# Kernel optimization log

Hardware: AMD Instinct MI355X
Metric: run time of the kernel (lower is better)

## Reference

```python
import jax, jax.numpy as jnp
import numpy as np

H, KV, D, HID = 16, 4, 64, 1024
OUT_MIN, OUT_MAX = 32, 8192  # output_size_max = config.max_position_embeddings


def _score_attn(x, Wq, Wk, Wv, Wo):
    # Full (non-causal, unmasked) GQA attention whose o_proj maps to 1 scalar/token.
    B, S, _ = x.shape
    q = (x @ Wq).reshape(B, S, H, D)
    k = jnp.repeat((x @ Wk).reshape(B, S, KV, D), H // KV, axis=2)  # repeat_kv
    v = jnp.repeat((x @ Wv).reshape(B, S, KV, D), H // KV, axis=2)
    scores = jnp.einsum('bqhd,bkhd->bhqk', q, k) / jnp.asarray(np.sqrt(D), x.dtype)
    a = jax.nn.softmax(scores, axis=-1)
    o = jnp.einsum('bhqk,bkhd->bqhd', a, v).reshape(B, S, H * D)
    return o @ Wo  # (B, S, 1)


def _dynamic_sizes(x, Wq, Wk, Wv, Wo, scale):
    s = _score_attn(x, Wq, Wk, Wv, Wo)               # (B,S,1)
    means = jax.nn.sigmoid(s).mean(axis=1)            # (B,1) (no attention_mask)
    sizes = means.squeeze(-1) * scale * (OUT_MAX - OUT_MIN) + OUT_MIN
    return sizes.astype(jnp.int32)                    # torch .int() truncation


def _segment_ids(sizes_np, S, max_len):
    # torch.linspace(0, L, sz+1).long() boundaries; token t -> segment i with
    # intervals[i] <= t < intervals[i+1]; right-aligned into [max_len] per batch.
    B = len(sizes_np)
    seg = np.zeros((B, S), np.int32)
    t = np.arange(S)
    for b, sz in enumerate(sizes_np):
        sz = int(sz)
        bnd = np.floor(np.linspace(0.0, S, sz + 1, dtype=np.float64)).astype(np.int64)
        s = np.clip(np.searchsorted(bnd, t, side='right') - 1, 0, sz - 1)
        seg[b] = b * max_len + (max_len - sz) + s
    return jnp.asarray(seg)


def setup_inputs() -> dict:
    key = jax.random.key(0)
    ks = jax.random.split(key, 10)
    B, S = 4, 2048
    x = jax.random.normal(ks[0], (B, S, HID), jnp.float32)
    def lin(k, i, o):
        return jax.random.normal(k, (i, o), jnp.float32) / np.sqrt(i).astype(np.float32)
    return dict(
        hidden_states=x,
        Wq1=lin(ks[1], HID, H * D), Wk1=lin(ks[2], HID, KV * D),
        Wv1=lin(ks[3], HID, KV * D), Wo1=lin(ks[4], H * D, 1),
        Wq2=lin(ks[5], HID, H * D), Wk2=lin(ks[6], HID, KV * D),
        Wv2=lin(ks[7], HID, KV * D), Wo2=lin(ks[8], H * D, 1),
        scale_param=jnp.asarray(0.01, jnp.float32),
    )


def reference(hidden_states, Wq1, Wk1, Wv1, Wo1, Wq2, Wk2, Wv2, Wo2, scale_param):
    B, S, Hd = hidden_states.shape
    # 1) size-estimation attention -> per-batch dynamic output sizes (data-dependent shape)
    sizes = _dynamic_sizes(hidden_states, Wq1, Wk1, Wv1, Wo1, scale_param)
    sizes_np = np.asarray(jax.device_get(sizes))
    max_len = int(sizes_np.max())
    seg = _segment_ids(sizes_np, S, max_len)          # (B,S) global segment ids
    # 2) weighted-pooling attention -> per-token sigmoid weights
    w = jax.nn.sigmoid(_score_attn(hidden_states, Wq2, Wk2, Wv2, Wo2)).squeeze(-1)  # (B,S)
    # 3) weighted average pooling over dynamic-size segments (vectorized scatter-add)
    num = jax.ops.segment_sum((hidden_states * w[..., None]).reshape(B * S, Hd),
                              seg.reshape(-1), num_segments=B * max_len)
    den = jax.ops.segment_sum(w.reshape(-1), seg.reshape(-1), num_segments=B * max_len)
    pooled = (num / (den[:, None] + 1e-8)).reshape(B, max_len, Hd)
    out_mask = jnp.arange(max_len)[None, :] >= (max_len - sizes)[:, None]
    return pooled, out_mask, sizes
```

## Files before the change

### kernel.cpp

```cpp
#include <hip/hip_runtime.h>
#include <math.h>

#define TB 256

constexpr int B_ = 4, S_ = 2048, HID_ = 1024, H_ = 16, KV_ = 4, D_ = 64;

typedef short sh8 __attribute__((ext_vector_type(8)));
typedef float fl4 __attribute__((ext_vector_type(4)));
typedef unsigned short u16;
typedef unsigned int u32;

__device__ __forceinline__ u16 f2bf(float f) {
  u32 u = __float_as_uint(f);
  u += 0x7fff + ((u >> 16) & 1);
  return (u16)(u >> 16);
}
__device__ __forceinline__ float bf2f(u16 h) { return __uint_as_float(((u32)h) << 16); }

constexpr size_t XSZ   = (size_t)B_ * S_ * HID_;
constexpr size_t WQH_O = 2 * XSZ;
constexpr size_t WQSZ  = (size_t)2 * HID_ * (H_ * D_);
constexpr size_t WQL_O = WQH_O + WQSZ;
constexpr size_t WKH_O = WQH_O + 2 * WQSZ;
constexpr size_t WKSZ  = (size_t)2 * HID_ * (KV_ * D_);
constexpr size_t WKL_O = WKH_O + WKSZ;
constexpr size_t KH_O  = WKH_O + 2 * WKSZ;
constexpr size_t KSZ   = (size_t)2 * B_ * KV_ * S_ * D_;
constexpr size_t KL_O  = KH_O + KSZ;
constexpr size_t KPLANE = (size_t)S_ * D_;
constexpr size_t FBASE   = (KH_O + 2 * KSZ) / 2;
constexpr size_t U_OFF   = FBASE;
constexpr size_t U_SZ    = (size_t)2 * B_ * H_ * S_;
constexpr size_t WVO_OFF = U_OFF + U_SZ;
constexpr size_t WVO_SZ  = (size_t)HID_ * 32;
constexpr size_t SH_OFF  = WVO_OFF + WVO_SZ;
constexpr size_t SH_SZ   = (size_t)2 * B_ * S_ * H_;
constexpr size_t W_OFF   = SH_OFF + SH_SZ;
constexpr size_t W_SZ    = (size_t)B_ * S_;
constexpr size_t SUM_OFF = W_OFF + W_SZ;
constexpr size_t SIZES_OFF = SUM_OFF + 8;

__global__ __launch_bounds__(TB) void conv_x_kernel(
    const float* __restrict__ x, float* __restrict__ ws) {
  u16* XH = (u16*)ws;
  u16* XL = XH + XSZ;
  int bt = blockIdx.x;
  int tid = threadIdx.x, w = tid >> 6, lane = tid & 63, quad = lane >> 4, col = lane & 15;
  int b = bt >> 7, t16 = bt & 127;
  const float* row = x + ((size_t)b * S_ + t16 * 16 + col) * HID_;
#pragma unroll
  for (int i = 0; i < 8; ++i) {
    int cs = w + i * 4;
    const float* src = row + cs * 32 + quad * 8;
    float4 v0 = *reinterpret_cast<const float4*>(src);
    float4 v1 = *reinterpret_cast<const float4*>(src + 4);
    float vv[8] = {v0.x, v0.y, v0.z, v0.w, v1.x, v1.y, v1.z, v1.w};
    sh8 hh, ll;
#pragma unroll
    for (int j = 0; j < 8; ++j) {
      u16 hb = f2bf(vv[j]);
      hh[j] = (short)hb;
      ll[j] = (short)f2bf(vv[j] - bf2f(hb));
    }
    size_t fb = ((size_t)bt * 32 + cs) * 512 + (size_t)lane * 8;
    *reinterpret_cast<sh8*>(XH + fb) = hh;
    *reinterpret_cast<sh8*>(XL + fb) = ll;
  }
}

__global__ __launch_bounds__(TB) void conv_w_kernel(
    const float* __restrict__ W1, const float* __restrict__ W2,
    u16* __restrict__ OH, u16* __restrict__ OL, int ncols) {
  __shared__ float wt[32][257];
  int ngrp = ncols >> 8;
  int blk = blockIdx.x;
  int a = blk / (32 * ngrp);
  int rem = blk - a * 32 * ngrp;
  int cs = rem / ngrp, ng = rem - cs * ngrp;
  const float* W = a ? W2 : W1;
  int tid = threadIdx.x;
#pragma unroll
  for (int i = 0; i < 8; ++i) {
    int e = tid + i * 256;
    int r = e >> 6, c4 = (e & 63) * 4;
    float4 v = *reinterpret_cast<const float4*>(
        W + ((size_t)(cs * 32 + r)) * ncols + ng * 256 + c4);
    wt[r][c4] = v.x; wt[r][c4 + 1] = v.y; wt[r][c4 + 2] = v.z; wt[r][c4 + 3] = v.w;
  }
  __syncthreads();
  int w = tid >> 6, lane = tid & 63, quad = lane >> 4, col = lane & 15;
  int NF = ncols >> 4;
#pragma unroll
  for (int f = 0; f < 4; ++f) {
    int n16 = w * 4 + f;
    sh8 hh, ll;
#pragma unroll
    for (int j = 0; j < 8; ++j) {
      float v = wt[quad * 8 + j][n16 * 16 + col];
      u16 hb = f2bf(v);
      hh[j] = (short)hb;
      ll[j] = (short)f2bf(v - bf2f(hb));
    }
    size_t fb = (((size_t)a * 32 + cs) * NF + ng * 16 + n16) * 512 + (size_t)lane * 8;
    *reinterpret_cast<sh8*>(OH + fb) = hh;
    *reinterpret_cast<sh8*>(OL + fb) = ll;
  }
}

__global__ __launch_bounds__(TB) void wvo_kernel(
    const float* __restrict__ Wv1, const float* __restrict__ Wo1,
    const float* __restrict__ Wv2, const float* __restrict__ Wo2,
    float* __restrict__ ws) {
  int n = blockIdx.x;
  int a = n >> 4, h = n & 15, kv = h >> 2;
  const float* Wv = a ? Wv2 : Wv1;
  const float* Wo = a ? Wo2 : Wo1;
  for (int c = threadIdx.x; c < HID_; c += TB) {
    const float* vr = Wv + (size_t)c * (KV_ * D_) + kv * D_;
    const float* wo = Wo + h * D_;
    float acc = 0.f;
#pragma unroll 16
    for (int d = 0; d < D_; ++d) acc += vr[d] * wo[d];
    ws[WVO_OFF + (size_t)c * 32 + n] = acc;
  }
}

__global__ __launch_bounds__(TB) void k_gemm_kernel(float* __restrict__ ws) {
  __shared__ __align__(16) float xs[64][68];
  int k0 = blockIdx.x * 64;
  int kv = blockIdx.y;
  int ab = blockIdx.z, a = ab >> 2, b = ab & 3;
  int tid = threadIdx.x, w = tid >> 6, lane = tid & 63, quad = lane >> 4, col = lane & 15;
  const u16* XH = (const u16*)ws;
  const u16* XL = XH + XSZ;
  const u16* WKH = XH + WKH_O;
  const u16* WKL = XH + WKL_O;
  int tq = (w & 1) * 2, nq = (w >> 1) * 2;
  fl4 C[2][2] = {};
#pragma unroll 2
  for (int cs = 0; cs < 32; ++cs) {
    sh8 ah[2], al[2], bh[2], bl[2];
#pragma unroll
    for (int ti = 0; ti < 2; ++ti) {
      size_t fb = (((size_t)b * 128 + (k0 >> 4) + tq + ti) * 32 + cs) * 512 + (size_t)lane * 8;
      ah[ti] = *reinterpret_cast<const sh8*>(XH + fb);
      if (a == 0) al[ti] = *reinterpret_cast<const sh8*>(XL + fb);
    }
#pragma unroll
    for (int ni = 0; ni < 2; ++ni) {
      size_t fb = (((size_t)a * 32 + cs) * 16 + kv * 4 + nq + ni) * 512 + (size_t)lane * 8;
      bh[ni] = *reinterpret_cast<const sh8*>(WKH + fb);
      if (a == 0) bl[ni] = *reinterpret_cast<const sh8*>(WKL + fb);
    }
#pragma unroll
    for (int ti = 0; ti < 2; ++ti)
#pragma unroll
      for (int ni = 0; ni < 2; ++ni) {
        C[ti][ni] = __builtin_amdgcn_mfma_f32_16x16x32_bf16(ah[ti], bh[ni], C[ti][ni], 0, 0, 0);
        if (a == 0) {
          C[ti][ni] = __builtin_amdgcn_mfma_f32_16x16x32_bf16(al[ti], bh[ni], C[ti][ni], 0, 0, 0);
          C[ti][ni] = __builtin_amdgcn_mfma_f32_16x16x32_bf16(ah[ti], bl[ni], C[ti][ni], 0, 0, 0);
        }
      }
  }
#pragma unroll
  for (int ti = 0; ti < 2; ++ti)
#pragma unroll
    for (int ni = 0; ni < 2; ++ni)
#pragma unroll
      for (int r = 0; r < 4; ++r)
        xs[(tq + ti) * 16 + quad * 4 + r][(nq + ni) * 16 + col] = C[ti][ni][r];
  __syncthreads();
  u16* KH = (u16*)ws + KH_O;
  u16* KL = (u16*)ws + KL_O;
  size_t plane = (size_t)((a * B_ + b) * KV_ + kv) * KPLANE;
#pragma unroll
  for (int t = 0; t < 2; ++t) {
    int f = w + t * 4;
    int k16 = f & 3, ds = f >> 2;
    const float* row = &xs[k16 * 16 + col][ds * 32 + quad * 8];
    sh8 hh, ll;
#pragma unroll
    for (int j = 0; j < 8; ++j) {
      float v = row[j];
      u16 hb = f2bf(v);
      hh[j] = (short)hb;
      ll[j] = (short)f2bf(v - bf2f(hb));
    }
    size_t fb = plane + ((size_t)(((k0 >> 4) + k16) * 2 + ds)) * 512 + (size_t)lane * 8;
    *reinterpret_cast<sh8*>(KH + fb) = hh;
    if (a == 0) *reinterpret_cast<sh8*>(KL + fb) = ll;
  }
}

__global__ __launch_bounds__(TB) void u_gemm_kernel(
    const float* __restrict__ x, float* __restrict__ ws) {
  __shared__ float xs[64][68];
  __shared__ float uw[64][36];
  int k0 = blockIdx.x * 64, b = blockIdx.y;
  int tid = threadIdx.x;
  int tk = tid >> 2, ng = tid & 3;
  int lr = tid >> 4, lc4 = (tid & 15) * 4;
  float acc[8] = {};
  for (int c0 = 0; c0 < HID_; c0 += 64) {
    __syncthreads();
#pragma unroll
    for (int p = 0; p < 4; ++p) {
      int r = lr + p * 16;
      *reinterpret_cast<float4*>(&xs[r][lc4]) =
          *reinterpret_cast<const float4*>(x + ((size_t)(b * S_ + k0 + r) * HID_ + c0 + lc4));
    }
    {
      int cc = tid >> 3, n4 = (tid & 7) * 4;
      *reinterpret_cast<float4*>(&uw[cc][n4]) =
          *reinterpret_cast<const float4*>(ws + WVO_OFF + (size_t)(c0 + cc) * 32 + n4);
      *reinterpret_cast<float4*>(&uw[cc + 32][n4]) =
          *reinterpret_cast<const float4*>(ws + WVO_OFF + (size_t)(c0 + cc + 32) * 32 + n4);
    }
    __syncthreads();
#pragma unroll 8
    for (int cc = 0; cc < 64; ++cc) {
      float xv = xs[tk][cc];
      float4 a0 = *reinterpret_cast<const float4*>(&uw[cc][ng * 8]);
      float4 a1 = *reinterpret_cast<const float4*>(&uw[cc][ng * 8 + 4]);
      acc[0] += xv * a0.x; acc[1] += xv * a0.y; acc[2] += xv * a0.z; acc[3] += xv * a0.w;
      acc[4] += xv * a1.x; acc[5] += xv * a1.y; acc[6] += xv * a1.z; acc[7] += xv * a1.w;
    }
  }
#pragma unroll
  for (int j = 0; j < 8; ++j) {
    int n = ng * 8 + j, a = n >> 4, h = n & 15;
    ws[U_OFF + ((size_t)(a * B_ + b) * H_ + h) * S_ + k0 + tk] = acc[j];
  }
}

__global__ __launch_bounds__(TB) void attn_kernel(float* __restrict__ ws) {
  __shared__ __align__(16) float Qt[64][68];
  __shared__ __align__(16) u16 kbuf[16 * 512];
  int q0 = blockIdx.x * 64;
  int ah = blockIdx.y, a = ah >> 4, h = ah & 15, kv = h >> 2;
  int b = blockIdx.z;
  int tid = threadIdx.x, w = tid >> 6, lane = tid & 63, quad = lane >> 4, col = lane & 15;
  const u16* XH = (const u16*)ws;
  const u16* XL = XH + XSZ;
  const u16* WQH = XH + WQH_O;
  const u16* WQL = XH + WQL_O;

  {
    int tq = (w & 1) * 2, nq = (w >> 1) * 2;
    fl4 C[2][2] = {};
#pragma unroll 2
    for (int cs = 0; cs < 32; ++cs) {
      sh8 ah_[2], al_[2], bh_[2], bl_[2];
#pragma unroll
      for (int ti = 0; ti < 2; ++ti) {
        size_t fb = (((size_t)b * 128 + (q0 >> 4) + tq + ti) * 32 + cs) * 512 + (size_t)lane * 8;
        ah_[ti] = *reinterpret_cast<const sh8*>(XH + fb);
        if (a == 0) al_[ti] = *reinterpret_cast<const sh8*>(XL + fb);
      }
#pragma unroll
      for (int ni = 0; ni < 2; ++ni) {
        size_t fb = (((size_t)a * 32 + cs) * 64 + h * 4 + nq + ni) * 512 + (size_t)lane * 8;
        bh_[ni] = *reinterpret_cast<const sh8*>(WQH + fb);
        if (a == 0) bl_[ni] = *reinterpret_cast<const sh8*>(WQL + fb);
      }
#pragma unroll
      for (int ti = 0; ti < 2; ++ti)
#pragma unroll
        for (int ni = 0; ni < 2; ++ni) {
          C[ti][ni] = __builtin_amdgcn_mfma_f32_16x16x32_bf16(ah_[ti], bh_[ni], C[ti][ni], 0, 0, 0);
          if (a == 0) {
            C[ti][ni] = __builtin_amdgcn_mfma_f32_16x16x32_bf16(al_[ti], bh_[ni], C[ti][ni], 0, 0, 0);
            C[ti][ni] = __builtin_amdgcn_mfma_f32_16x16x32_bf16(ah_[ti], bl_[ni], C[ti][ni], 0, 0, 0);
          }
        }
    }
#pragma unroll
    for (int ti = 0; ti < 2; ++ti)
#pragma unroll
      for (int ni = 0; ni < 2; ++ni)
#pragma unroll
        for (int r = 0; r < 4; ++r)
          Qt[(nq + ni) * 16 + col][(tq + ti) * 16 + quad * 4 + r] = C[ti][ni][r];
  }
  __syncthreads();

  sh8 qh[2], ql[2];
#pragma unroll
  for (int ds = 0; ds < 2; ++ds)
#pragma unroll
    for (int j = 0; j < 8; ++j) {
      float v = Qt[ds * 32 + quad * 8 + j][w * 16 + col];
      u16 hb = f2bf(v);
      qh[ds][j] = (short)hb;
      if (a == 0) ql[ds][j] = (short)f2bf(v - bf2f(hb));
    }

  const u16* KHg = (const u16*)ws + KH_O + (size_t)((a * B_ + b) * KV_ + kv) * KPLANE;
  const u16* KLg = (const u16*)ws + KL_O + (size_t)((a * B_ + b) * KV_ + kv) * KPLANE;
  const float* Ug = ws + U_OFF + ((size_t)(a * B_ + b) * H_ + h) * S_;
  int nld = (a == 0) ? 4 : 2;
  float num[4] = {}, den[4] = {};
  for (int k0 = 0; k0 < S_; k0 += 64) {
    __syncthreads();
#pragma unroll
    for (int i = 0; i < 4; ++i) {
      if (i < nld) {
        int c = tid + TB * i, f = c >> 6, ln = c & 63;
        const u16* src;
        if (a == 0) {
          int st = f >> 2, ds = (f >> 1) & 1, p = f & 1;
          src = (p ? KLg : KHg) + ((size_t)(((k0 >> 4) + st) * 2 + ds)) * 512 + (size_t)ln * 8;
        } else {
          int st = f >> 1, ds = f & 1;
          src = KHg + ((size_t)(((k0 >> 4) + st) * 2 + ds)) * 512 + (size_t)ln * 8;
        }
        *reinterpret_cast<uint4*>(kbuf + (size_t)c * 8) = *reinterpret_cast<const uint4*>(src);
      }
    }
    __syncthreads();
    const sh8* kb = (const sh8*)kbuf;
#pragma unroll
    for (int st = 0; st < 4; ++st) {
      sh8 bh0, bh1, bl0, bl1;
      if (a == 0) {
        bh0 = kb[(st * 4 + 0) * 64 + lane];
        bl0 = kb[(st * 4 + 1) * 64 + lane];
        bh1 = kb[(st * 4 + 2) * 64 + lane];
        bl1 = kb[(st * 4 + 3) * 64 + lane];
      } else {
        bh0 = kb[(st * 2 + 0) * 64 + lane];
        bh1 = kb[(st * 2 + 1) * 64 + lane];
      }
      fl4 C = {0.f, 0.f, 0.f, 0.f};
      C = __builtin_amdgcn_mfma_f32_16x16x32_bf16(qh[0], bh0, C, 0, 0, 0);
      C = __builtin_amdgcn_mfma_f32_16x16x32_bf16(qh[1], bh1, C, 0, 0, 0);
      if (a == 0) {
        C = __builtin_amdgcn_mfma_f32_16x16x32_bf16(ql[0], bh0, C, 0, 0, 0);
        C = __builtin_amdgcn_mfma_f32_16x16x32_bf16(ql[1], bh1, C, 0, 0, 0);
        C = __builtin_amdgcn_mfma_f32_16x16x32_bf16(qh[0], bl0, C, 0, 0, 0);
        C = __builtin_amdgcn_mfma_f32_16x16x32_bf16(qh[1], bl1, C, 0, 0, 0);
      }
      float uval = Ug[k0 + st * 16 + col];
#pragma unroll
      for (int r = 0; r < 4; ++r) {
        float e = __expf(C[r] * 0.125f);
        den[r] += e;
        num[r] += e * uval;
      }
    }
  }
#pragma unroll
  for (int off = 1; off < 16; off <<= 1)
#pragma unroll
    for (int r = 0; r < 4; ++r) {
      den[r] += __shfl_xor(den[r], off);
      num[r] += __shfl_xor(num[r], off);
    }
  if (col == 0) {
#pragma unroll
    for (int r = 0; r < 4; ++r) {
      int q = q0 + w * 16 + quad * 4 + r;
      ws[SH_OFF + ((size_t)(a * B_ + b) * S_ + q) * H_ + h] = num[r] / den[r];
    }
  }
}

__global__ __launch_bounds__(TB) void post_kernel(float* __restrict__ ws) {
  int g = blockIdx.x * TB + threadIdx.x;
  int b = g >> 11, q = g & (S_ - 1);
  const float* sh = ws + SH_OFF;
  float s1 = 0.f, s2 = 0.f;
#pragma unroll
  for (int h = 0; h < H_; ++h) {
    s1 += sh[((size_t)b * S_ + q) * H_ + h];
    s2 += sh[((size_t)(B_ + b) * S_ + q) * H_ + h];
  }
  ws[W_OFF + g] = 1.f / (1.f + expf(-s2));
  double sig = 1.0 / (1.0 + exp(-(double)s1));
#pragma unroll
  for (int off = 1; off < 64; off <<= 1) sig += __shfl_xor(sig, off);
  __shared__ double red[4];
  int tid = threadIdx.x;
  if ((tid & 63) == 0) red[tid >> 6] = sig;
  __syncthreads();
  if (tid == 0)
    atomicAdd(reinterpret_cast<double*>(ws + SUM_OFF) + b,
              red[0] + red[1] + red[2] + red[3]);
}

__global__ void sizes_kernel(const float* __restrict__ scale_p, float* __restrict__ ws,
                             float* __restrict__ out_sizes) {
  int b = threadIdx.x;
  if (b < B_) {
    double m = reinterpret_cast<const double*>(ws + SUM_OFF)[b] / (double)S_;
    double v = m * (double)(*scale_p) * (double)(8192 - 32) + 32.0;
    int sz = (int)v;
    reinterpret_cast<int*>(ws + SIZES_OFF)[b] = sz;
    out_sizes[b] = (float)sz;
  }
}

__global__ __launch_bounds__(TB) void pool_kernel(
    const float* __restrict__ x, const float* __restrict__ ws,
    float* __restrict__ out, int max_len) {
  int p = blockIdx.x, b = blockIdx.y;
  int sz = reinterpret_cast<const int*>(ws + SIZES_OFF)[b];
  int s = p - (max_len - sz);
  int tid = threadIdx.x;
  size_t obase = ((size_t)b * max_len + p) * HID_;
  size_t maskbase = (size_t)B_ * max_len * HID_;
  if (s < 0) {
    *reinterpret_cast<float4*>(out + obase + tid * 4) = make_float4(0.f, 0.f, 0.f, 0.f);
    if (tid == 0) out[maskbase + (size_t)b * max_len + p] = 0.f;
    return;
  }
  double step = (double)S_ / (double)sz;
  int t0 = (int)floor((double)s * step);
  int t1 = (s + 1 == sz) ? S_ : (int)floor((double)(s + 1) * step);
  const float* wv = ws + W_OFF + (size_t)b * S_;
  const float* xb = x + (size_t)b * S_ * HID_;
  float den = 0.f, acc0 = 0.f, acc1 = 0.f, acc2 = 0.f, acc3 = 0.f;
  for (int t = t0; t < t1; ++t) {
    float wt = wv[t];
    den += wt;
    float4 xv = *reinterpret_cast<const float4*>(xb + (size_t)t * HID_ + tid * 4);
    acc0 += xv.x * wt; acc1 += xv.y * wt; acc2 += xv.z * wt; acc3 += xv.w * wt;
  }
  float d = den + 1e-8f;
  *reinterpret_cast<float4*>(out + obase + tid * 4) =
      make_float4(acc0 / d, acc1 / d, acc2 / d, acc3 / d);
  if (tid == 0) out[maskbase + (size_t)b * max_len + p] = 1.f;
}

extern "C" void kernel_launch(void* const* d_in, const int* in_sizes, int n_in,
                              void* d_out, int out_size, void* d_ws, size_t ws_size,
                              hipStream_t stream) {
  const float* x    = (const float*)d_in[0];
  const float* Wq1  = (const float*)d_in[1];
  const float* Wk1  = (const float*)d_in[2];
  const float* Wv1  = (const float*)d_in[3];
  const float* Wo1  = (const float*)d_in[4];
  const float* Wq2  = (const float*)d_in[5];
  const float* Wk2  = (const float*)d_in[6];
  const float* Wv2  = (const float*)d_in[7];
  const float* Wo2  = (const float*)d_in[8];
  const float* scale = (const float*)d_in[9];
  float* ws  = (float*)d_ws;
  u16* wsu   = (u16*)d_ws;
  float* out = (float*)d_out;

  int max_len = (out_size - B_) / (B_ * (HID_ + 1));

  hipMemsetAsync((void*)(ws + SUM_OFF), 0, 4 * sizeof(double), stream);
  conv_x_kernel<<<B_ * (S_ / 16), TB, 0, stream>>>(x, ws);
  conv_w_kernel<<<2 * 32 * 4, TB, 0, stream>>>(Wq1, Wq2, wsu + WQH_O, wsu + WQL_O, H_ * D_);
  conv_w_kernel<<<2 * 32 * 1, TB, 0, stream>>>(Wk1, Wk2, wsu + WKH_O, wsu + WKL_O, KV_ * D_);
  wvo_kernel<<<32, TB, 0, stream>>>(Wv1, Wo1, Wv2, Wo2, ws);
  k_gemm_kernel<<<dim3(S_ / 64, KV_, 8), TB, 0, stream>>>(ws);
  u_gemm_kernel<<<dim3(S_ / 64, B_), TB, 0, stream>>>(x, ws);
  attn_kernel<<<dim3(S_ / 64, 32, B_), TB, 0, stream>>>(ws);
  post_kernel<<<(B_ * S_) / TB, TB, 0, stream>>>(ws);
  float* out_sizes = out + (size_t)B_ * max_len * HID_ + (size_t)B_ * max_len;
  sizes_kernel<<<1, 64, 0, stream>>>(scale, ws, out_sizes);
  pool_kernel<<<dim3(max_len, B_), TB, 0, stream>>>(x, ws, out, max_len);
}
```

Baseline: 510.7 us.

## Merge prep kernels into two launches, fold sizes into pool, hoist attn addressing

```diff
diff --git a/kernel.cpp b/kernel.cpp
--- a/kernel.cpp
+++ b/kernel.cpp
@@ -38,47 +38,16 @@
 constexpr size_t W_OFF   = SH_OFF + SH_SZ;
 constexpr size_t W_SZ    = (size_t)B_ * S_;
 constexpr size_t SUM_OFF = W_OFF + W_SZ;
-constexpr size_t SIZES_OFF = SUM_OFF + 8;
-
-__global__ __launch_bounds__(TB) void conv_x_kernel(
-    const float* __restrict__ x, float* __restrict__ ws) {
-  u16* XH = (u16*)ws;
-  u16* XL = XH + XSZ;
-  int bt = blockIdx.x;
-  int tid = threadIdx.x, w = tid >> 6, lane = tid & 63, quad = lane >> 4, col = lane & 15;
-  int b = bt >> 7, t16 = bt & 127;
-  const float* row = x + ((size_t)b * S_ + t16 * 16 + col) * HID_;
-#pragma unroll
-  for (int i = 0; i < 8; ++i) {
-    int cs = w + i * 4;
-    const float* src = row + cs * 32 + quad * 8;
-    float4 v0 = *reinterpret_cast<const float4*>(src);
-    float4 v1 = *reinterpret_cast<const float4*>(src + 4);
-    float vv[8] = {v0.x, v0.y, v0.z, v0.w, v1.x, v1.y, v1.z, v1.w};
-    sh8 hh, ll;
-#pragma unroll
-    for (int j = 0; j < 8; ++j) {
-      u16 hb = f2bf(vv[j]);
-      hh[j] = (short)hb;
-      ll[j] = (short)f2bf(vv[j] - bf2f(hb));
-    }
-    size_t fb = ((size_t)bt * 32 + cs) * 512 + (size_t)lane * 8;
-    *reinterpret_cast<sh8*>(XH + fb) = hh;
-    *reinterpret_cast<sh8*>(XL + fb) = ll;
-  }
-}
-
-__global__ __launch_bounds__(TB) void conv_w_kernel(
+
+__device__ __forceinline__ void conv_w_body(
     const float* __restrict__ W1, const float* __restrict__ W2,
-    u16* __restrict__ OH, u16* __restrict__ OL, int ncols) {
-  __shared__ float wt[32][257];
+    u16* __restrict__ OH, u16* __restrict__ OL, int ncols,
+    int blk, int tid, float wt[32][257]) {
   int ngrp = ncols >> 8;
-  int blk = blockIdx.x;
   int a = blk / (32 * ngrp);
   int rem = blk - a * 32 * ngrp;
   int cs = rem / ngrp, ng = rem - cs * ngrp;
   const float* W = a ? W2 : W1;
-  int tid = threadIdx.x;
 #pragma unroll
   for (int i = 0; i < 8; ++i) {
     int e = tid + i * 256;
@@ -107,136 +76,173 @@
   }
 }
 
-__global__ __launch_bounds__(TB) void wvo_kernel(
+__global__ __launch_bounds__(TB) void prep1_kernel(
+    const float* __restrict__ x,
+    const float* __restrict__ Wq1, const float* __restrict__ Wq2,
+    const float* __restrict__ Wk1, const float* __restrict__ Wk2,
     const float* __restrict__ Wv1, const float* __restrict__ Wo1,
     const float* __restrict__ Wv2, const float* __restrict__ Wo2,
     float* __restrict__ ws) {
-  int n = blockIdx.x;
-  int a = n >> 4, h = n & 15, kv = h >> 2;
-  const float* Wv = a ? Wv2 : Wv1;
-  const float* Wo = a ? Wo2 : Wo1;
-  for (int c = threadIdx.x; c < HID_; c += TB) {
-    const float* vr = Wv + (size_t)c * (KV_ * D_) + kv * D_;
-    const float* wo = Wo + h * D_;
-    float acc = 0.f;
+  __shared__ float wt[32][257];
+  int blk = blockIdx.x, tid = threadIdx.x;
+  u16* wsu = (u16*)ws;
+  if (blk < 512) {
+    u16* XH = wsu;
+    u16* XL = XH + XSZ;
+    int bt = blk;
+    int w = tid >> 6, lane = tid & 63, quad = lane >> 4, col = lane & 15;
+    int b = bt >> 7, t16 = bt & 127;
+    const float* row = x + ((size_t)b * S_ + t16 * 16 + col) * HID_;
+#pragma unroll
+    for (int i = 0; i < 8; ++i) {
+      int cs = w + i * 4;
+      const float* src = row + cs * 32 + quad * 8;
+      float4 v0 = *reinterpret_cast<const float4*>(src);
+      float4 v1 = *reinterpret_cast<const float4*>(src + 4);
+      float vv[8] = {v0.x, v0.y, v0.z, v0.w, v1.x, v1.y, v1.z, v1.w};
+      sh8 hh, ll;
+#pragma unroll
+      for (int j = 0; j < 8; ++j) {
+        u16 hb = f2bf(vv[j]);
+        hh[j] = (short)hb;
+        ll[j] = (short)f2bf(vv[j] - bf2f(hb));
+      }
+      size_t fb = ((size_t)bt * 32 + cs) * 512 + (size_t)lane * 8;
+      *reinterpret_cast<sh8*>(XH + fb) = hh;
+      *reinterpret_cast<sh8*>(XL + fb) = ll;
+    }
+  } else if (blk < 768) {
+    conv_w_body(Wq1, Wq2, wsu + WQH_O, wsu + WQL_O, H_ * D_, blk - 512, tid, wt);
+  } else if (blk < 832) {
+    conv_w_body(Wk1, Wk2, wsu + WKH_O, wsu + WKL_O, KV_ * D_, blk - 768, tid, wt);
+  } else {
+    int n = blk - 832, a = n >> 4, h = n & 15, kv = h >> 2;
+    const float* Wv = a ? Wv2 : Wv1;
+    const float* Wo = a ? Wo2 : Wo1;
+    for (int c = tid; c < HID_; c += TB) {
+      const float* vr = Wv + (size_t)c * (KV_ * D_) + kv * D_;
+      const float* wo = Wo + h * D_;
+      float acc = 0.f;
 #pragma unroll 16
-    for (int d = 0; d < D_; ++d) acc += vr[d] * wo[d];
-    ws[WVO_OFF + (size_t)c * 32 + n] = acc;
-  }
-}
-
-__global__ __launch_bounds__(TB) void k_gemm_kernel(float* __restrict__ ws) {
+      for (int d = 0; d < D_; ++d) acc += vr[d] * wo[d];
+      ws[WVO_OFF + (size_t)c * 32 + n] = acc;
+    }
+  }
+}
+
+__global__ __launch_bounds__(TB) void prep2_kernel(
+    const float* __restrict__ x, float* __restrict__ ws) {
   __shared__ __align__(16) float xs[64][68];
-  int k0 = blockIdx.x * 64;
-  int kv = blockIdx.y;
-  int ab = blockIdx.z, a = ab >> 2, b = ab & 3;
-  int tid = threadIdx.x, w = tid >> 6, lane = tid & 63, quad = lane >> 4, col = lane & 15;
-  const u16* XH = (const u16*)ws;
-  const u16* XL = XH + XSZ;
-  const u16* WKH = XH + WKH_O;
-  const u16* WKL = XH + WKL_O;
-  int tq = (w & 1) * 2, nq = (w >> 1) * 2;
-  fl4 C[2][2] = {};
+  __shared__ float uw[64][36];
+  int blk = blockIdx.x, tid = threadIdx.x;
+  if (blk < 1024) {
+    int k0 = (blk & 31) * 64;
+    int kv = (blk >> 5) & 3;
+    int ab = blk >> 7, a = ab >> 2, b = ab & 3;
+    int w = tid >> 6, lane = tid & 63, quad = lane >> 4, col = lane & 15;
+    const u16* XH = (const u16*)ws;
+    const u16* XL = XH + XSZ;
+    const u16* WKH = XH + WKH_O;
+    const u16* WKL = XH + WKL_O;
+    int tq = (w & 1) * 2, nq = (w >> 1) * 2;
+    fl4 C[2][2] = {};
 #pragma unroll 2
-  for (int cs = 0; cs < 32; ++cs) {
-    sh8 ah[2], al[2], bh[2], bl[2];
-#pragma unroll
-    for (int ti = 0; ti < 2; ++ti) {
-      size_t fb = (((size_t)b * 128 + (k0 >> 4) + tq + ti) * 32 + cs) * 512 + (size_t)lane * 8;
-      ah[ti] = *reinterpret_cast<const sh8*>(XH + fb);
-      if (a == 0) al[ti] = *reinterpret_cast<const sh8*>(XL + fb);
-    }
-#pragma unroll
-    for (int ni = 0; ni < 2; ++ni) {
-      size_t fb = (((size_t)a * 32 + cs) * 16 + kv * 4 + nq + ni) * 512 + (size_t)lane * 8;
-      bh[ni] = *reinterpret_cast<const sh8*>(WKH + fb);
-      if (a == 0) bl[ni] = *reinterpret_cast<const sh8*>(WKL + fb);
+    for (int cs = 0; cs < 32; ++cs) {
+      sh8 ah[2], al[2], bh[2], bl[2];
+#pragma unroll
+      for (int ti = 0; ti < 2; ++ti) {
+        size_t fb = (((size_t)b * 128 + (k0 >> 4) + tq + ti) * 32 + cs) * 512 + (size_t)lane * 8;
+        ah[ti] = *reinterpret_cast<const sh8*>(XH + fb);
+        if (a == 0) al[ti] = *reinterpret_cast<const sh8*>(XL + fb);
+      }
+#pragma unroll
+      for (int ni = 0; ni < 2; ++ni) {
+        size_t fb = (((size_t)a * 32 + cs) * 16 + kv * 4 + nq + ni) * 512 + (size_t)lane * 8;
+        bh[ni] = *reinterpret_cast<const sh8*>(WKH + fb);
+        if (a == 0) bl[ni] = *reinterpret_cast<const sh8*>(WKL + fb);
+      }
+#pragma unroll
+      for (int ti = 0; ti < 2; ++ti)
+#pragma unroll
+        for (int ni = 0; ni < 2; ++ni) {
+          C[ti][ni] = __builtin_amdgcn_mfma_f32_16x16x32_bf16(ah[ti], bh[ni], C[ti][ni], 0, 0, 0);
+          if (a == 0) {
+            C[ti][ni] = __builtin_amdgcn_mfma_f32_16x16x32_bf16(al[ti], bh[ni], C[ti][ni], 0, 0, 0);
+            C[ti][ni] = __builtin_amdgcn_mfma_f32_16x16x32_bf16(ah[ti], bl[ni], C[ti][ni], 0, 0, 0);
+          }
+        }
     }
 #pragma unroll
     for (int ti = 0; ti < 2; ++ti)
 #pragma unroll
-      for (int ni = 0; ni < 2; ++ni) {
-        C[ti][ni] = __builtin_amdgcn_mfma_f32_16x16x32_bf16(ah[ti], bh[ni], C[ti][ni], 0, 0, 0);
-        if (a == 0) {
-          C[ti][ni] = __builtin_amdgcn_mfma_f32_16x16x32_bf16(al[ti], bh[ni], C[ti][ni], 0, 0, 0);
-          C[ti][ni] = __builtin_amdgcn_mfma_f32_16x16x32_bf16(ah[ti], bl[ni], C[ti][ni], 0, 0, 0);
-        }
-      }
-  }
-#pragma unroll
-  for (int ti = 0; ti < 2; ++ti)
-#pragma unroll
-    for (int ni = 0; ni < 2; ++ni)
-#pragma unroll
-      for (int r = 0; r < 4; ++r)
-        xs[(tq + ti) * 16 + quad * 4 + r][(nq + ni) * 16 + col] = C[ti][ni][r];
-  __syncthreads();
-  u16* KH = (u16*)ws + KH_O;
-  u16* KL = (u16*)ws + KL_O;
-  size_t plane = (size_t)((a * B_ + b) * KV_ + kv) * KPLANE;
-#pragma unroll
-  for (int t = 0; t < 2; ++t) {
-    int f = w + t * 4;
-    int k16 = f & 3, ds = f >> 2;
-    const float* row = &xs[k16 * 16 + col][ds * 32 + quad * 8];
-    sh8 hh, ll;
+      for (int ni = 0; ni < 2; ++ni)
+#pragma unroll
+        for (int r = 0; r < 4; ++r)
+          xs[(tq + ti) * 16 + quad * 4 + r][(nq + ni) * 16 + col] = C[ti][ni][r];
+    __syncthreads();
+    u16* KH = (u16*)ws + KH_O;
+    u16* KL = (u16*)ws + KL_O;
+    size_t plane = (size_t)((a * B_ + b) * KV_ + kv) * KPLANE;
+#pragma unroll
+    for (int t = 0; t < 2; ++t) {
+      int f = w + t * 4;
+      int k16 = f & 3, ds = f >> 2;
+      const float* row = &xs[k16 * 16 + col][ds * 32 + quad * 8];
+      sh8 hh, ll;
+#pragma unroll
+      for (int j = 0; j < 8; ++j) {
+        float v = row[j];
+        u16 hb = f2bf(v);
+        hh[j] = (short)hb;
+        ll[j] = (short)f2bf(v - bf2f(hb));
+      }
+      size_t fb = plane + ((size_t)(((k0 >> 4) + k16) * 2 + ds)) * 512 + (size_t)lane * 8;
+      *reinterpret_cast<sh8*>(KH + fb) = hh;
+      if (a == 0) *reinterpret_cast<sh8*>(KL + fb) = ll;
+    }
+  } else {
+    int i = blk - 1024;
+    int k0 = (i & 31) * 64, b = i >> 5;
+    int tk = tid >> 2, ng = tid & 3;
+    int lr = tid >> 4, lc4 = (tid & 15) * 4;
+    float acc[8] = {};
+    for (int c0 = 0; c0 < HID_; c0 += 64) {
+      __syncthreads();
+#pragma unroll
+      for (int p = 0; p < 4; ++p) {
+        int r = lr + p * 16;
+        *reinterpret_cast<float4*>(&xs[r][lc4]) =
+            *reinterpret_cast<const float4*>(x + ((size_t)(b * S_ + k0 + r) * HID_ + c0 + lc4));
+      }
+      {
+        int cc = tid >> 3, n4 = (tid & 7) * 4;
+        *reinterpret_cast<float4*>(&uw[cc][n4]) =
+            *reinterpret_cast<const float4*>(ws + WVO_OFF + (size_t)(c0 + cc) * 32 + n4);
+        *reinterpret_cast<float4*>(&uw[cc + 32][n4]) =
+            *reinterpret_cast<const float4*>(ws + WVO_OFF + (size_t)(c0 + cc + 32) * 32 + n4);
+      }
+      __syncthreads();
+#pragma unroll 8
+      for (int cc = 0; cc < 64; ++cc) {
+        float xv = xs[tk][cc];
+        float4 a0 = *reinterpret_cast<const float4*>(&uw[cc][ng * 8]);
+        float4 a1 = *reinterpret_cast<const float4*>(&uw[cc][ng * 8 + 4]);
+        acc[0] += xv * a0.x; acc[1] += xv * a0.y; acc[2] += xv * a0.z; acc[3] += xv * a0.w;
+        acc[4] += xv * a1.x; acc[5] += xv * a1.y; acc[6] += xv * a1.z; acc[7] += xv * a1.w;
+      }
+    }
 #pragma unroll
     for (int j = 0; j < 8; ++j) {
-      float v = row[j];
-      u16 hb = f2bf(v);
-      hh[j] = (short)hb;
-      ll[j] = (short)f2bf(v - bf2f(hb));
-    }
-    size_t fb = plane + ((size_t)(((k0 >> 4) + k16) * 2 + ds)) * 512 + (size_t)lane * 8;
-    *reinterpret_cast<sh8*>(KH + fb) = hh;
-    if (a == 0) *reinterpret_cast<sh8*>(KL + fb) = ll;
-  }
-}
-
-__global__ __launch_bounds__(TB) void u_gemm_kernel(
-    const float* __restrict__ x, float* __restrict__ ws) {
-  __shared__ float xs[64][68];
-  __shared__ float uw[64][36];
-  int k0 = blockIdx.x * 64, b = blockIdx.y;
-  int tid = threadIdx.x;
-  int tk = tid >> 2, ng = tid & 3;
-  int lr = tid >> 4, lc4 = (tid & 15) * 4;
-  float acc[8] = {};
-  for (int c0 = 0; c0 < HID_; c0 += 64) {
-    __syncthreads();
-#pragma unroll
-    for (int p = 0; p < 4; ++p) {
-      int r = lr + p * 16;
-      *reinterpret_cast<float4*>(&xs[r][lc4]) =
-          *reinterpret_cast<const float4*>(x + ((size_t)(b * S_ + k0 + r) * HID_ + c0 + lc4));
-    }
-    {
-      int cc = tid >> 3, n4 = (tid & 7) * 4;
-      *reinterpret_cast<float4*>(&uw[cc][n4]) =
-          *reinterpret_cast<const float4*>(ws + WVO_OFF + (size_t)(c0 + cc) * 32 + n4);
-      *reinterpret_cast<float4*>(&uw[cc + 32][n4]) =
-          *reinterpret_cast<const float4*>(ws + WVO_OFF + (size_t)(c0 + cc + 32) * 32 + n4);
-    }
-    __syncthreads();
-#pragma unroll 8
-    for (int cc = 0; cc < 64; ++cc) {
-      float xv = xs[tk][cc];
-      float4 a0 = *reinterpret_cast<const float4*>(&uw[cc][ng * 8]);
-      float4 a1 = *reinterpret_cast<const float4*>(&uw[cc][ng * 8 + 4]);
-      acc[0] += xv * a0.x; acc[1] += xv * a0.y; acc[2] += xv * a0.z; acc[3] += xv * a0.w;
-      acc[4] += xv * a1.x; acc[5] += xv * a1.y; acc[6] += xv * a1.z; acc[7] += xv * a1.w;
-    }
-  }
-#pragma unroll
-  for (int j = 0; j < 8; ++j) {
-    int n = ng * 8 + j, a = n >> 4, h = n & 15;
-    ws[U_OFF + ((size_t)(a * B_ + b) * H_ + h) * S_ + k0 + tk] = acc[j];
+      int n = ng * 8 + j, a = n >> 4, h = n & 15;
+      ws[U_OFF + ((size_t)(a * B_ + b) * H_ + h) * S_ + k0 + tk] = acc[j];
+    }
   }
 }
 
 __global__ __launch_bounds__(TB) void attn_kernel(float* __restrict__ ws) {
-  __shared__ __align__(16) float Qt[64][68];
-  __shared__ __align__(16) u16 kbuf[16 * 512];
+  __shared__ __align__(16) char smem[64 * 68 * 4];
+  float (*Qt)[68] = reinterpret_cast<float(*)[68]>(smem);
+  u16* kbuf = reinterpret_cast<u16*>(smem);
   int q0 = blockIdx.x * 64;
   int ah = blockIdx.y, a = ah >> 4, h = ah & 15, kv = h >> 2;
   int b = blockIdx.z;
@@ -298,27 +304,36 @@
 
   const u16* KHg = (const u16*)ws + KH_O + (size_t)((a * B_ + b) * KV_ + kv) * KPLANE;
   const u16* KLg = (const u16*)ws + KL_O + (size_t)((a * B_ + b) * KV_ + kv) * KPLANE;
-  const float* Ug = ws + U_OFF + ((size_t)(a * B_ + b) * H_ + h) * S_;
   int nld = (a == 0) ? 4 : 2;
+  const u16* srcp[4];
+#pragma unroll
+  for (int i = 0; i < 4; ++i) {
+    if (i < nld) {
+      int c = tid + TB * i, f = c >> 6, ln = c & 63;
+      if (a == 0) {
+        int st = f >> 2, ds = (f >> 1) & 1, p = f & 1;
+        srcp[i] = (p ? KLg : KHg) + ((size_t)(st * 2 + ds)) * 512 + (size_t)ln * 8;
+      } else {
+        int st = f >> 1, ds = f & 1;
+        srcp[i] = KHg + ((size_t)(st * 2 + ds)) * 512 + (size_t)ln * 8;
+      }
+    }
+  }
+  const float* up = ws + U_OFF + ((size_t)(a * B_ + b) * H_ + h) * S_ + col;
   float num[4] = {}, den[4] = {};
-  for (int k0 = 0; k0 < S_; k0 += 64) {
+  for (int kt = 0; kt < 32; ++kt) {
     __syncthreads();
 #pragma unroll
-    for (int i = 0; i < 4; ++i) {
+    for (int i = 0; i < 4; ++i)
       if (i < nld) {
-        int c = tid + TB * i, f = c >> 6, ln = c & 63;
-        const u16* src;
-        if (a == 0) {
-          int st = f >> 2, ds = (f >> 1) & 1, p = f & 1;
-          src = (p ? KLg : KHg) + ((size_t)(((k0 >> 4) + st) * 2 + ds)) * 512 + (size_t)ln * 8;
-        } else {
-          int st = f >> 1, ds = f & 1;
-          src = KHg + ((size_t)(((k0 >> 4) + st) * 2 + ds)) * 512 + (size_t)ln * 8;
-        }
-        *reinterpret_cast<uint4*>(kbuf + (size_t)c * 8) = *reinterpret_cast<const uint4*>(src);
-      }
-    }
+        *reinterpret_cast<uint4*>(kbuf + (size_t)(tid + TB * i) * 8) =
+            *reinterpret_cast<const uint4*>(srcp[i]);
+        srcp[i] += 4096;
+      }
     __syncthreads();
+    float u0 = up[0], u1 = up[16], u2 = up[32], u3 = up[48];
+    up += 64;
+    float uv[4] = {u0, u1, u2, u3};
     const sh8* kb = (const sh8*)kbuf;
 #pragma unroll
     for (int st = 0; st < 4; ++st) {
@@ -341,12 +356,11 @@
         C = __builtin_amdgcn_mfma_f32_16x16x32_bf16(qh[0], bl0, C, 0, 0, 0);
         C = __builtin_amdgcn_mfma_f32_16x16x32_bf16(qh[1], bl1, C, 0, 0, 0);
       }
-      float uval = Ug[k0 + st * 16 + col];
 #pragma unroll
       for (int r = 0; r < 4; ++r) {
         float e = __expf(C[r] * 0.125f);
         den[r] += e;
-        num[r] += e * uval;
+        num[r] += e * uv[st];
       }
     }
   }
@@ -389,27 +403,19 @@
               red[0] + red[1] + red[2] + red[3]);
 }
 
-__global__ void sizes_kernel(const float* __restrict__ scale_p, float* __restrict__ ws,
-                             float* __restrict__ out_sizes) {
-  int b = threadIdx.x;
-  if (b < B_) {
-    double m = reinterpret_cast<const double*>(ws + SUM_OFF)[b] / (double)S_;
-    double v = m * (double)(*scale_p) * (double)(8192 - 32) + 32.0;
-    int sz = (int)v;
-    reinterpret_cast<int*>(ws + SIZES_OFF)[b] = sz;
-    out_sizes[b] = (float)sz;
-  }
-}
-
 __global__ __launch_bounds__(TB) void pool_kernel(
-    const float* __restrict__ x, const float* __restrict__ ws,
-    float* __restrict__ out, int max_len) {
+    const float* __restrict__ x, const float* __restrict__ scale_p,
+    const float* __restrict__ ws, float* __restrict__ out, int max_len) {
   int p = blockIdx.x, b = blockIdx.y;
-  int sz = reinterpret_cast<const int*>(ws + SIZES_OFF)[b];
+  double m = reinterpret_cast<const double*>(ws + SUM_OFF)[b] / (double)S_;
+  double v = m * (double)(*scale_p) * (double)(8192 - 32) + 32.0;
+  int sz = (int)v;
   int s = p - (max_len - sz);
   int tid = threadIdx.x;
   size_t obase = ((size_t)b * max_len + p) * HID_;
   size_t maskbase = (size_t)B_ * max_len * HID_;
+  size_t sizebase = maskbase + (size_t)B_ * max_len;
+  if (p == 0 && tid == 0) out[sizebase + b] = (float)sz;
   if (s < 0) {
     *reinterpret_cast<float4*>(out + obase + tid * 4) = make_float4(0.f, 0.f, 0.f, 0.f);
     if (tid == 0) out[maskbase + (size_t)b * max_len + p] = 0.f;
@@ -447,21 +453,14 @@
   const float* Wo2  = (const float*)d_in[8];
   const float* scale = (const float*)d_in[9];
   float* ws  = (float*)d_ws;
-  u16* wsu   = (u16*)d_ws;
   float* out = (float*)d_out;
 
   int max_len = (out_size - B_) / (B_ * (HID_ + 1));
 
   hipMemsetAsync((void*)(ws + SUM_OFF), 0, 4 * sizeof(double), stream);
-  conv_x_kernel<<<B_ * (S_ / 16), TB, 0, stream>>>(x, ws);
-  conv_w_kernel<<<2 * 32 * 4, TB, 0, stream>>>(Wq1, Wq2, wsu + WQH_O, wsu + WQL_O, H_ * D_);
-  conv_w_kernel<<<2 * 32 * 1, TB, 0, stream>>>(Wk1, Wk2, wsu + WKH_O, wsu + WKL_O, KV_ * D_);
-  wvo_kernel<<<32, TB, 0, stream>>>(Wv1, Wo1, Wv2, Wo2, ws);
-  k_gemm_kernel<<<dim3(S_ / 64, KV_, 8), TB, 0, stream>>>(ws);
-  u_gemm_kernel<<<dim3(S_ / 64, B_), TB, 0, stream>>>(x, ws);
+  prep1_kernel<<<864, TB, 0, stream>>>(x, Wq1, Wq2, Wk1, Wk2, Wv1, Wo1, Wv2, Wo2, ws);
+  prep2_kernel<<<1152, TB, 0, stream>>>(x, ws);
   attn_kernel<<<dim3(S_ / 64, 32, B_), TB, 0, stream>>>(ws);
   post_kernel<<<(B_ * S_) / TB, TB, 0, stream>>>(ws);
-  float* out_sizes = out + (size_t)B_ * max_len * HID_ + (size_t)B_ * max_len;
-  sizes_kernel<<<1, 64, 0, stream>>>(scale, ws, out_sizes);
-  pool_kernel<<<dim3(max_len, B_), TB, 0, stream>>>(x, ws, out, max_len);
-}
+  pool_kernel<<<dim3(max_len, B_), TB, 0, stream>>>(x, scale, ws, out, max_len);
+}
```

Measured after the change: 499.9 us. 2.1% less time.
